# Kernel optimization log

Hardware: AMD Instinct MI355X
Metric: run time of the kernel (lower is better)

Reference implementation:

```python
import jax, jax.numpy as jnp
import numpy as np

NUM_BASE = 92
NUM_NOVEL = 40
GAMMA = 2.0
ALPHA = 0.25
DISTIL_FACTOR = 1.0
BSZ, N_DET, DIM_FEAT, DIM_HID, DIM_EMB = 16, 48, 2048, 1024, 512
EMB_HALF = DIM_EMB // 2


def _pair_ids(n):
    # all ordered pairs (i, j), i != j  (trajid2pairid)
    s, o = np.meshgrid(np.arange(n), np.arange(n), indexing='ij')
    m = s != o
    return s[m].astype(np.int32), o[m].astype(np.int32)


def _norm(x, eps=1e-12):
    # F.normalize(dim=-1)
    return x / jnp.maximum(jnp.linalg.norm(x, axis=-1, keepdims=True), eps)


def _sigmoid_focal_loss(logits, targets):
    # torchvision.ops.sigmoid_focal_loss, alpha=0.25, gamma=2, reduction='none'
    p = jax.nn.sigmoid(logits)
    ce = jnp.maximum(logits, 0) - logits * targets + jnp.log1p(jnp.exp(-jnp.abs(logits)))
    p_t = p * targets + (1.0 - p) * (1.0 - targets)
    loss = ce * (1.0 - p_t) ** GAMMA
    a_t = ALPHA * targets + (1.0 - ALPHA) * (1.0 - targets)
    return a_t * loss


def setup_inputs() -> dict:
    key = jax.random.key(0)
    ks = jax.random.split(key, 12)
    sids_np, oids_np = _pair_ids(N_DET)
    P = sids_np.shape[0]  # 2256 pairs per video
    w = lambda k, shape, s=0.02: jax.random.normal(k, shape, dtype=jnp.float32) * s
    return {
        'det_feats': jax.random.normal(ks[0], (BSZ, N_DET, DIM_FEAT), dtype=jnp.float32),
        'traj_embds': jax.random.normal(ks[1], (BSZ, N_DET, EMB_HALF), dtype=jnp.float32),
        'relpos_feats': jax.random.normal(ks[2], (BSZ, P, 12), dtype=jnp.float32),
        'classifier_weights': _norm(jax.random.normal(ks[3], (NUM_BASE, DIM_EMB), dtype=jnp.float32)) / np.sqrt(2.0),
        'W1': w(ks[4], (2 * DIM_FEAT, DIM_HID)), 'b1': jnp.zeros((DIM_HID,), jnp.float32),
        'W2': w(ks[5], (DIM_HID, DIM_HID)), 'b2': jnp.zeros((DIM_HID,), jnp.float32),
        'W3': w(ks[6], (DIM_HID, DIM_EMB)),
        'R1': w(ks[7], (12, 256), 0.1), 'rb1': jnp.zeros((256,), jnp.float32),
        'R2': w(ks[8], (256, DIM_EMB), 0.1),
        'temperature': jnp.full((1,), 0.02, dtype=jnp.float32),
        'labels': jax.random.randint(ks[9], (BSZ, P, 1 + NUM_BASE + NUM_NOVEL), 0, 2, dtype=jnp.int32),
        'sids': jnp.asarray(sids_np),
        'oids': jnp.asarray(oids_np),
    }


def reference(det_feats, traj_embds, relpos_feats, classifier_weights,
              W1, b1, W2, b2, W3, R1, rb1, R2, temperature,
              labels, sids, oids):
    Df = det_feats.shape[-1]
    De = traj_embds.shape[-1]
    # gather subject / object features for all pairs, flatten batch
    s_f = det_feats[:, sids, :].reshape(-1, Df)   # [N, Df]
    o_f = det_feats[:, oids, :].reshape(-1, Df)
    so = jnp.concatenate([s_f, o_f], axis=-1)      # [N, 2*Df]
    # trajpair_proj MLP
    h = jax.nn.relu(so @ W1 + b1)
    h = jax.nn.relu(h @ W2 + b2)
    so_proj = h @ W3                                # [N, dim_emb]
    so_n = _norm(so_proj)
    # relpos branch
    rp = relpos_feats.reshape(-1, relpos_feats.shape[-1])
    re = jax.nn.relu(rp @ R1 + rb1) @ R2
    re = _norm(re)
    combined = _norm(so_n + re)
    logits = (combined @ classifier_weights.T) / temperature  # [N, num_base]
    # cls_loss_on_base
    lab = labels.reshape(-1, 1 + NUM_BASE + NUM_NOVEL).astype(logits.dtype)
    pos_mask = jnp.any(lab[:, 1:1 + NUM_BASE] > 0, axis=-1)
    neg_mask = lab[:, 0] > 0
    lab_base = lab[:, 1:1 + NUM_BASE]
    fl_pos = _sigmoid_focal_loss(logits, lab_base)
    pos_den = jnp.maximum(pos_mask.sum(), 1).astype(logits.dtype) * NUM_BASE
    pos_loss = jnp.sum(fl_pos * pos_mask[:, None]) / pos_den
    fl_neg = _sigmoid_focal_loss(logits, jnp.zeros_like(logits))
    neg_den = jnp.maximum(neg_mask.sum(), 1).astype(logits.dtype) * NUM_BASE
    neg_loss = jnp.sum(fl_neg * neg_mask[:, None]) / neg_den
    # distillation L1 loss
    s_e = traj_embds[:, sids, :].reshape(-1, De)
    o_e = traj_embds[:, oids, :].reshape(-1, De)
    distil_target = jnp.concatenate([s_e, o_e], axis=-1)  # [N, dim_emb]
    distil_loss = jnp.mean(jnp.abs(distil_target - so_proj)) * DISTIL_FACTOR
    total_loss = pos_loss + neg_loss + distil_loss
    return total_loss
```

## Files before the change

### kernel.cpp

```cpp
#include <hip/hip_runtime.h>
#include <math.h>

constexpr int BSZ   = 16;
constexpr int NDET  = 48;
constexpr int PAIRS = NDET * (NDET - 1);
constexpr int ROWS  = BSZ * PAIRS;
constexpr int DF    = 2048;
constexpr int DH    = 1024;
constexpr int DE    = 512;
constexpr int EHALF = 256;
constexpr int NCLS  = 92;
constexpr int NEXT  = DE + 128;
constexpr int LABW  = 1 + 92 + 40;

typedef __attribute__((ext_vector_type(8))) short bf16x8;
typedef __attribute__((ext_vector_type(4))) float f32x4;

__device__ __forceinline__ short f2bf(float f) {
    union { float f; unsigned u; } a; a.f = f;
    unsigned r = a.u + 0x7fffu + ((a.u >> 16) & 1u);
    return (short)(r >> 16);
}
__device__ __forceinline__ float bf2f(short h) {
    union { unsigned u; float f; } x;
    x.u = ((unsigned)(unsigned short)h) << 16;
    return x.f;
}

constexpr int N4DET = BSZ * NDET * DF / 4;
constexpr int N4CWT = 128 * DE / 4;
constexpr int N4W3  = DH * DE / 4;
constexpr int N4R2  = 256 * DE / 4;
constexpr int NCONVB = (N4DET + N4CWT + N4W3 + N4R2) / 256;

struct TransJobs {
    const float* src[5];
    short*       dst[5];
    int K[5], N[5];
    int cum[6];
};

__global__ __launch_bounds__(256) void prep_kernel(
    const float* __restrict__ det, short* __restrict__ det_bf,
    const float* __restrict__ cw, short* __restrict__ cwt,
    const float* __restrict__ W3, short* __restrict__ W3bf,
    const float* __restrict__ R2, short* __restrict__ R2bf,
    TransJobs jobs)
{
    if (blockIdx.x < NCONVB) {
        int i = blockIdx.x * 256 + threadIdx.x;
        const float* src; short* dst; int k;
        if (i < N4DET) { src = det; dst = det_bf; k = i; }
        else if (i < N4DET + N4CWT) {
            k = i - N4DET;
            int n = (k * 4) >> 9;
            short4 o = {0, 0, 0, 0};
            if (n < NCLS) {
                float4 v = ((const float4*)cw)[k];
                o.x = f2bf(v.x); o.y = f2bf(v.y); o.z = f2bf(v.z); o.w = f2bf(v.w);
            }
            ((short4*)cwt)[k] = o;
            return;
        }
        else if (i < N4DET + N4CWT + N4W3) { src = W3; dst = W3bf; k = i - N4DET - N4CWT; }
        else { src = R2; dst = R2bf; k = i - N4DET - N4CWT - N4W3; }
        float4 v = ((const float4*)src)[k];
        short4 o;
        o.x = f2bf(v.x); o.y = f2bf(v.y); o.z = f2bf(v.z); o.w = f2bf(v.w);
        ((short4*)dst)[k] = o;
        return;
    }
    __shared__ float tile[32][33];
    int t = blockIdx.x - NCONVB;
    int j = 0;
    while (t >= jobs.cum[j + 1]) ++j;
    int lt = t - jobs.cum[j];
    int K = jobs.K[j], N = jobs.N[j];
    int nx = N >> 5;
    int ky = lt / nx, nxi = lt - ky * nx;
    int n0 = nxi * 32, k0 = ky * 32;
    const float* src = jobs.src[j];
    short* dst = jobs.dst[j];
    int tx = threadIdx.x & 31, ty = threadIdx.x >> 5;
#pragma unroll
    for (int i = ty; i < 32; i += 8)
        tile[i][tx] = src[(size_t)(k0 + i) * N + n0 + tx];
    __syncthreads();
#pragma unroll
    for (int i = ty; i < 32; i += 8)
        dst[(size_t)(n0 + i) * K + k0 + tx] = f2bf(tile[tx][i]);
}

__device__ __forceinline__ void load16_lds(const void* g, void* l) {
    __builtin_amdgcn_global_load_lds(
        (const __attribute__((address_space(1))) unsigned int*)g,
        (__attribute__((address_space(3))) unsigned int*)l, 16, 0, 0);
}

template <bool BIAS, bool RELU, bool OUTBF16, bool SWIZZLE, bool DUAL>
__global__ __launch_bounds__(256, 4) void mfma_gemm(
    const short* __restrict__ A, const short* __restrict__ Bt,
    const float* __restrict__ bias, void* __restrict__ C,
    int M, int N, int K, int lda, int ldb,
    const short* A2, const short* Bt2, void* C2, int nsplit,
    int K2, int lda2, int ldb2, int N2)
{
    __shared__ __align__(16) char smem_raw[32768];
    short* As = (short*)smem_raw;
    short* Bs = As + 128 * 64;

    int bx, by;
    if (SWIZZLE) {
        int nb  = gridDim.x;
        int gid = blockIdx.y * nb + blockIdx.x;
        int xcd = gid & 7;
        int j   = gid >> 3;
        int rows_per = gridDim.y >> 3;
        int lr  = j / nb;
        bx = j - lr * nb;
        by = xcd * rows_per + lr;
    } else {
        bx = blockIdx.x; by = blockIdx.y;
    }
    if (DUAL && bx >= nsplit) {
        bx -= nsplit; A = A2; Bt = Bt2; C = C2;
        K = K2; lda = lda2; ldb = ldb2; N = N2;
    }
    if (by * 128 >= M) return;

    const int tid  = threadIdx.x;
    const int wave = tid >> 6;
    const int lane = tid & 63;
    const int m0 = by * 128;
    const int n0 = bx * 128;
    const int wm = (wave & 1) * 64;
    const int wn = (wave >> 1) * 64;

    f32x4 acc[4][4] = {};

    const int q  = lane >> 4;
    const int lm = lane & 15;

    for (int k0 = 0; k0 < K; k0 += 64) {
#pragma unroll
        for (int it = 0; it < 4; ++it) {
            int c    = (it & 1) * 256 + tid;
            int half = it >> 1;
            int row  = c >> 2;
            int kk   = (c & 3) * 8 + half * 32;
            int ldsc = half * 4096 + ((it & 1) * 256 + wave * 64) * 8;
            int gm = m0 + row; if (gm >= M) gm = M - 1;
            load16_lds(A + (size_t)gm * lda + k0 + kk, As + ldsc);
            int gn = n0 + row;
            load16_lds(Bt + (size_t)gn * ldb + k0 + kk, Bs + ldsc);
        }
        __syncthreads();

#pragma unroll
        for (int half = 0; half < 2; ++half) {
            const short* Ah = As + half * 4096;
            const short* Bh = Bs + half * 4096;
            bf16x8 af[4], bfr[4];
#pragma unroll
            for (int t = 0; t < 4; ++t) {
                af[t]  = *(const bf16x8*)(Ah + (wm + t * 16 + lm) * 32 + q * 8);
                bfr[t] = *(const bf16x8*)(Bh + (wn + t * 16 + lm) * 32 + q * 8);
            }
#pragma unroll
            for (int tm = 0; tm < 4; ++tm)
#pragma unroll
                for (int tn = 0; tn < 4; ++tn)
                    acc[tm][tn] = __builtin_amdgcn_mfma_f32_16x16x32_bf16(
                        af[tm], bfr[tn], acc[tm][tn], 0, 0, 0);
        }
        __syncthreads();
    }

    if (OUTBF16) {
        float* scratch = (float*)smem_raw + wave * (16 * 68);
#pragma unroll
        for (int tm = 0; tm < 4; ++tm) {
            __syncthreads();
#pragma unroll
            for (int tn = 0; tn < 4; ++tn) {
                float bv = BIAS ? bias[n0 + wn + tn * 16 + lm] : 0.0f;
#pragma unroll
                for (int r = 0; r < 4; ++r) {
                    float v = acc[tm][tn][r] + bv;
                    if (RELU) v = fmaxf(v, 0.0f);
                    scratch[(q * 4 + r) * 68 + tn * 16 + lm] = v;
                }
            }
            __syncthreads();
#pragma unroll
            for (int p = 0; p < 2; ++p) {
                int row16 = (lane >> 3) + p * 8;
                int c0 = (lane & 7) * 8;
                float4 v0 = *(float4*)&scratch[row16 * 68 + c0];
                float4 v1 = *(float4*)&scratch[row16 * 68 + c0 + 4];
                bf16x8 o;
                o[0] = f2bf(v0.x); o[1] = f2bf(v0.y); o[2] = f2bf(v0.z); o[3] = f2bf(v0.w);
                o[4] = f2bf(v1.x); o[5] = f2bf(v1.y); o[6] = f2bf(v1.z); o[7] = f2bf(v1.w);
                int grow = m0 + wm + tm * 16 + row16;
                if (grow < M)
                    *(bf16x8*)((short*)C + (size_t)grow * N + n0 + wn + c0) = o;
            }
        }
    } else {
#pragma unroll
        for (int tm = 0; tm < 4; ++tm)
#pragma unroll
            for (int tn = 0; tn < 4; ++tn) {
                int col = n0 + wn + tn * 16 + lm;
#pragma unroll
                for (int r = 0; r < 4; ++r) {
                    int row = m0 + wm + tm * 16 + q * 4 + r;
                    if (row < M) {
                        float v = acc[tm][tn][r];
                        if (BIAS) v += bias[col];
                        if (RELU) v = fmaxf(v, 0.0f);
                        ((float*)C)[(size_t)row * N + col] = v;
                    }
                }
            }
    }
}

constexpr int N4UV = BSZ * NDET * 2048 / 4;
__global__ __launch_bounds__(256) void uvmerge_kernel(
    short* __restrict__ UVa, const short* __restrict__ UVb,
    const float* __restrict__ b1)
{
    int i = blockIdx.x * 256 + threadIdx.x;
    if (i >= N4UV) return;
    short4 a = ((const short4*)UVa)[i];
    short4 b = ((const short4*)UVb)[i];
    int col4 = i & 511;
    float4 bb = {0.0f, 0.0f, 0.0f, 0.0f};
    if (col4 < 256) bb = ((const float4*)b1)[col4];
    short4 o;
    o.x = f2bf(bf2f(a.x) + bf2f(b.x) + bb.x);
    o.y = f2bf(bf2f(a.y) + bf2f(b.y) + bb.y);
    o.z = f2bf(bf2f(a.z) + bf2f(b.z) + bb.z);
    o.w = f2bf(bf2f(a.w) + bf2f(b.w) + bb.w);
    ((short4*)UVa)[i] = o;
}

__global__ __launch_bounds__(256) void pairs_rh_kernel(
    const short* __restrict__ UVs,
    const int* __restrict__ sids, const int* __restrict__ oids,
    short* __restrict__ h1,
    const float* __restrict__ rp, const float* __restrict__ R1,
    const float* __restrict__ rb1, short* __restrict__ rh, int b0)
{
    int r = blockIdx.x;
    int b = b0 + r / PAIRS;
    int p = r % PAIRS;
    int j = threadIdx.x;

    size_t soff = (size_t)(b * NDET + sids[p]) * 2048;
    size_t ooff = (size_t)(b * NDET + oids[p]) * 2048 + 1024;
    short4 a1 = ((const short4*)(UVs + soff))[j];
    short4 a3 = ((const short4*)(UVs + ooff))[j];
    short4 h;
    h.x = f2bf(fmaxf(bf2f(a1.x) + bf2f(a3.x), 0.0f));
    h.y = f2bf(fmaxf(bf2f(a1.y) + bf2f(a3.y), 0.0f));
    h.z = f2bf(fmaxf(bf2f(a1.z) + bf2f(a3.z), 0.0f));
    h.w = f2bf(fmaxf(bf2f(a1.w) + bf2f(a3.w), 0.0f));
    ((short4*)(h1 + (size_t)r * DH))[j] = h;

    int rg = b0 * PAIRS + r;
    const float* row = rp + (size_t)rg * 12;
    float acc = rb1[j];
#pragma unroll
    for (int k = 0; k < 12; ++k) acc = fmaf(row[k], R1[k * 256 + j], acc);
    rh[(size_t)r * 256 + j] = f2bf(fmaxf(acc, 0.0f));
}

__global__ __launch_bounds__(256) void rowprep_focal_kernel(
    const short* __restrict__ so_ext, const short* __restrict__ re_ext,
    const float* __restrict__ traj, const float* __restrict__ temperature,
    const int* __restrict__ sids, const int* __restrict__ oids,
    const int* __restrict__ labels,
    float4* __restrict__ pn, float* __restrict__ dist_arr, int b0)
{
    int wave = threadIdx.x >> 6, lane = threadIdx.x & 63;
    int r = blockIdx.x * 4 + wave;
    int rg = b0 * PAIRS + r;
    int b = b0 + r / PAIRS;
    int p = r % PAIRS;

    const short* srow = so_ext + (size_t)r * NEXT;
    const short* rrow = re_ext + (size_t)r * NEXT;
    bf16x8 sv = *(const bf16x8*)(srow + lane * 8);
    bf16x8 uv = *(const bf16x8*)(rrow + lane * 8);
    float s[8], u[8];
#pragma unroll
    for (int i = 0; i < 8; ++i) { s[i] = bf2f(sv[i]); u[i] = bf2f(uv[i]); }

    const float* tsrc = (lane < 32)
        ? (traj + (size_t)(b * NDET + sids[p]) * EHALF + lane * 8)
        : (traj + (size_t)(b * NDET + oids[p]) * EHALF + (lane - 32) * 8);
    float4 t0 = ((const float4*)tsrc)[0], t1 = ((const float4*)tsrc)[1];
    float t[8] = {t0.x, t0.y, t0.z, t0.w, t1.x, t1.y, t1.z, t1.w};

    float ss = 0.0f, sr = 0.0f, rho = 0.0f, sd = 0.0f;
#pragma unroll
    for (int i = 0; i < 8; ++i) {
        ss  += s[i] * s[i];
        sr  += u[i] * u[i];
        rho += s[i] * u[i];
        sd  += fabsf(t[i] - s[i]);
    }
#pragma unroll
    for (int m = 1; m < 64; m <<= 1) {
        ss  += __shfl_xor(ss, m);
        sr  += __shfl_xor(sr, m);
        rho += __shfl_xor(rho, m);
        sd  += __shfl_xor(sd, m);
    }
    float inv_s = 1.0f / fmaxf(sqrtf(ss), 1e-12f);
    float inv_r = 1.0f / fmaxf(sqrtf(sr), 1e-12f);
    float ncomb = sqrtf(fmaxf(2.0f + 2.0f * rho * inv_s * inv_r, 0.0f));
    float scale = 1.0f / (fmaxf(ncomb, 1e-12f) * temperature[0]);

    float flp = 0.0f, fln = 0.0f, fm = 0.0f;
    size_t labbase = (size_t)rg * LABW;
#pragma unroll
    for (int h = 0; h < 2; ++h) {
        int c = lane + h * 64;
        if (c < NCLS) {
            float l = (bf2f(srow[DE + c]) * inv_s + bf2f(rrow[DE + c]) * inv_r) * scale;
            int tl = labels[labbase + 1 + c];
            if (tl > 0) fm = 1.0f;
            float tf = (float)tl;
            float pr = 1.0f / (1.0f + expf(-l));
            float lg = log1pf(expf(-fabsf(l)));
            float ce = fmaxf(l, 0.0f) - l * tf + lg;
            float pt = pr * tf + (1.0f - pr) * (1.0f - tf);
            float om = 1.0f - pt;
            float at = 0.25f * tf + 0.75f * (1.0f - tf);
            flp += at * ce * om * om;
            float ce0 = fmaxf(l, 0.0f) + lg;
            fln += 0.75f * ce0 * pr * pr;
        }
    }
#pragma unroll
    for (int m = 1; m < 64; m <<= 1) {
        flp += __shfl_xor(flp, m);
        fln += __shfl_xor(fln, m);
        fm  += __shfl_xor(fm, m);
    }
    if (lane == 0) {
        int posf = (fm > 0.5f) ? 1 : 0;
        int negf = (labels[labbase] > 0) ? 1 : 0;
        pn[rg] = make_float4(posf ? flp : 0.0f, negf ? fln : 0.0f, 0.0f,
                             (float)(posf + 2 * negf));
        dist_arr[rg] = sd;
    }
}

struct RedRec { double sp, sn, sd; int cp, cn; };
constexpr int RED1 = 64;
constexpr int ROWS_PER_RED = ROWS / RED1;

__global__ __launch_bounds__(256) void reduce1_kernel(
    const float4* __restrict__ pn, const float* __restrict__ dist_arr,
    RedRec* __restrict__ scratch)
{
    int tid = threadIdx.x;
    int base = blockIdx.x * ROWS_PER_RED;
    double sp = 0.0, sn = 0.0, sd = 0.0;
    int cp = 0, cn = 0;
    for (int i = tid; i < ROWS_PER_RED; i += 256) {
        float4 v = pn[base + i];
        sp += (double)v.x; sn += (double)v.y; sd += (double)dist_arr[base + i];
        int f = (int)v.w;
        cp += f & 1; cn += (f >> 1) & 1;
    }
    __shared__ double A[256], B[256], C[256];
    __shared__ int I[256], J[256];
    A[tid] = sp; B[tid] = sn; C[tid] = sd; I[tid] = cp; J[tid] = cn;
    __syncthreads();
    for (int st = 128; st > 0; st >>= 1) {
        if (tid < st) { A[tid] += A[tid + st]; B[tid] += B[tid + st]; C[tid] += C[tid + st];
                        I[tid] += I[tid + st]; J[tid] += J[tid + st]; }
        __syncthreads();
    }
    if (tid == 0) {
        RedRec rec; rec.sp = A[0]; rec.sn = B[0]; rec.sd = C[0];
        rec.cp = I[0]; rec.cn = J[0];
        scratch[blockIdx.x] = rec;
    }
}

__global__ __launch_bounds__(64) void reduce2_kernel(
    const RedRec* __restrict__ scratch, float* __restrict__ out)
{
    int lane = threadIdx.x;
    RedRec rec = scratch[lane];
    double sp = rec.sp, sn = rec.sn, sd = rec.sd;
    int cp = rec.cp, cn = rec.cn;
#pragma unroll
    for (int m = 1; m < 64; m <<= 1) {
        sp += __shfl_xor(sp, m);
        sn += __shfl_xor(sn, m);
        sd += __shfl_xor(sd, m);
        cp += __shfl_xor(cp, m);
        cn += __shfl_xor(cn, m);
    }
    if (lane == 0) {
        int cpv = cp < 1 ? 1 : cp;
        int cnv = cn < 1 ? 1 : cn;
        out[0] = (float)(sp / ((double)cpv * NCLS) +
                         sn / ((double)cnv * NCLS) +
                         sd / ((double)ROWS * DE));
    }
}

static inline int pad8(int x) { return (x + 7) & ~7; }

extern "C" void kernel_launch(void* const* d_in, const int* in_sizes, int n_in,
                              void* d_out, int out_size, void* d_ws, size_t ws_size,
                              hipStream_t stream)
{
    const float* det    = (const float*)d_in[0];
    const float* traj   = (const float*)d_in[1];
    const float* relpos = (const float*)d_in[2];
    const float* cw     = (const float*)d_in[3];
    const float* W1     = (const float*)d_in[4];
    const float* b1     = (const float*)d_in[5];
    const float* W2     = (const float*)d_in[6];
    const float* b2     = (const float*)d_in[7];
    const float* W3     = (const float*)d_in[8];
    const float* R1     = (const float*)d_in[9];
    const float* rb1    = (const float*)d_in[10];
    const float* R2     = (const float*)d_in[11];
    const float* temp   = (const float*)d_in[12];
    const int*   labels = (const int*)d_in[13];
    const int*   sids   = (const int*)d_in[14];
    const int*   oids   = (const int*)d_in[15];
    float* out = (float*)d_out;

    char* ws = (char*)d_ws;
    size_t off = 0;
    auto carve = [&](size_t bytes) -> char* {
        char* p = ws + off;
        off = (off + bytes + 255) & ~(size_t)255;
        return p;
    };
    float4* pn       = (float4*)carve((size_t)ROWS * 16);
    float*  dist_arr = (float*)carve((size_t)ROWS * 4);
    short*  det_bf   = (short*)carve((size_t)BSZ * NDET * DF * 2);
    short*  W1t      = (short*)carve((size_t)2048 * 2048 * 2);
    short*  W2t      = (short*)carve((size_t)DH * DH * 2);
    short*  W3t      = (short*)carve((size_t)NEXT * DH * 2);
    short*  R2t      = (short*)carve((size_t)NEXT * 256 * 2);
    short*  cwt      = (short*)carve((size_t)128 * DE * 2);
    short*  W3bf     = (short*)carve((size_t)DH * DE * 2);
    short*  R2bf     = (short*)carve((size_t)256 * DE * 2);
    short*  UVa      = (short*)carve((size_t)BSZ * NDET * 2048 * 2);
    short*  UVb      = (short*)carve((size_t)BSZ * NDET * 2048 * 2);
    RedRec* red_scratch = (RedRec*)carve((size_t)RED1 * sizeof(RedRec));
    size_t fixed_off = off;

    int b_ch = 1;
    for (int cand : {16, 8, 4, 2, 1}) {
        size_t rows  = (size_t)cand * PAIRS;
        size_t bytes = fixed_off + rows * 2048 + 256 + rows * 2048 + 256
                     + rows * 512 + 256 + rows * 1280 + 256;
        if (bytes <= ws_size) { b_ch = cand; break; }
    }
    const int chunk_rows = b_ch * PAIRS;
    const int n_chunks = BSZ / b_ch;
    char* reg1 = carve((size_t)chunk_rows * 2048);
    char* reg2 = carve((size_t)chunk_rows * 2048);
    char* reg3 = carve((size_t)chunk_rows * 512);
    char* reg4 = carve((size_t)chunk_rows * 1280);

    short* h1     = (short*)reg1;
    short* h2     = (short*)reg2;
    short* so_ext = (short*)reg1;
    short* rh     = (short*)reg3;
    short* re_ext = (short*)reg4;

    TransJobs tj;
    tj.src[0] = W1;                    tj.dst[0] = W1t;                   tj.K[0] = DF;  tj.N[0] = DH;
    tj.src[1] = W1 + (size_t)DF * DH;  tj.dst[1] = W1t + (size_t)DH * DF; tj.K[1] = DF;  tj.N[1] = DH;
    tj.src[2] = W2;                    tj.dst[2] = W2t;                   tj.K[2] = DH;  tj.N[2] = DH;
    tj.src[3] = W3;                    tj.dst[3] = W3t;                   tj.K[3] = DH;  tj.N[3] = DE;
    tj.src[4] = R2;                    tj.dst[4] = R2t;                   tj.K[4] = 256; tj.N[4] = DE;
    tj.cum[0] = 0;
    for (int i = 0; i < 5; ++i)
        tj.cum[i + 1] = tj.cum[i] + (tj.K[i] / 32) * (tj.N[i] / 32);
    prep_kernel<<<NCONVB + tj.cum[5], 256, 0, stream>>>(
        det, det_bf, cw, cwt, W3, W3bf, R2, R2bf, tj);

    mfma_gemm<false, false, true, false, true>
        <<<dim3(10, 1), 256, 0, stream>>>(
        cwt, W3bf, nullptr, W3t + (size_t)512 * DH, 128, 1024, 512, 512, 512,
        cwt, R2bf, R2t + (size_t)512 * 256, 8, 512, 512, 512, 256);

    mfma_gemm<false, false, true, false, true>
        <<<dim3(32, 6), 256, 0, stream>>>(
        det_bf, W1t, nullptr, UVa, BSZ * NDET, 2048, 1024, 2048, 2048,
        det_bf + 1024, W1t + 1024, UVb, 16, 1024, 2048, 2048, 2048);

    uvmerge_kernel<<<(N4UV + 255) / 256, 256, 0, stream>>>(UVa, UVb, b1);

    const int mg  = (chunk_rows + 127) / 128;
    const int mgp = pad8(mg);

    for (int c = 0; c < n_chunks; ++c) {
        int b0 = c * b_ch;
        int r0 = b0 * PAIRS;

        pairs_rh_kernel<<<chunk_rows, 256, 0, stream>>>(
            UVa, sids, oids, h1, relpos, R1, rb1, rh, b0);

        mfma_gemm<true, true, true, true, false>
            <<<dim3(DH / 128, mgp), 256, 0, stream>>>(
            h1, W2t, b2, h2, chunk_rows, DH, DH, DH, DH,
            nullptr, nullptr, nullptr, 0, 0, 0, 0, 0);

        mfma_gemm<false, false, true, true, true>
            <<<dim3(10, mgp), 256, 0, stream>>>(
            h2, W3t, nullptr, so_ext, chunk_rows, NEXT, DH, DH, DH,
            rh, R2t, re_ext, 5, 256, 256, 256, NEXT);

        rowprep_focal_kernel<<<chunk_rows / 4, 256, 0, stream>>>(
            so_ext, re_ext, traj, temp, sids, oids, labels, pn, dist_arr, b0);
    }

    reduce1_kernel<<<RED1, 256, 0, stream>>>(pn, dist_arr, red_scratch);
    reduce2_kernel<<<1, 64, 0, stream>>>(red_scratch, out);
}
```

Measured before the change: 388.4 us.

## Merge setup GEMMs into one multi-job launch and widen pairs kernel per wave

Replaces the two separate setup GEMM launches (classifier-projection and the W1 split products) with a single grouped GEMM kernel that dispatches blocks to four jobs. Its epilogue stages results through LDS so bf16 output is written as 16-byte rows. The pairs/relpos kernel is also changed to handle one row per wave with 16-byte vector loads instead of one row per 256-thread block. This cuts launch count, lets the small GEMMs fill otherwise idle CUs, and widens memory accesses, at the cost of a runtime job-lookup loop and added epilogue synchronisation.

After: 367.3 us, median of 2. -5.4%, faster.

```diff
diff --git a/kernel.cpp b/kernel.cpp
--- a/kernel.cpp
+++ b/kernel.cpp
@@ -226,6 +226,102 @@
     }
 }
 
+struct GemmJobs {
+    const short* A[4]; const short* Bt[4]; short* C[4];
+    int M[4], N[4], K[4], lda[4], ldb[4];
+    int cum[5];
+};
+
+__global__ __launch_bounds__(256, 4) void mfma_gemm_multi(GemmJobs jobs)
+{
+    __shared__ __align__(16) char smem_raw[32768];
+    short* As = (short*)smem_raw;
+    short* Bs = As + 128 * 64;
+
+    int bid = blockIdx.x;
+    int j = 0;
+    while (bid >= jobs.cum[j + 1]) ++j;
+    int lt = bid - jobs.cum[j];
+    const short* A  = jobs.A[j];
+    const short* Bt = jobs.Bt[j];
+    short* C = jobs.C[j];
+    int M = jobs.M[j], N = jobs.N[j], K = jobs.K[j];
+    int lda = jobs.lda[j], ldb = jobs.ldb[j];
+    int ncols = N >> 7;
+    int by = lt / ncols;
+    int bx = lt - by * ncols;
+
+    const int tid  = threadIdx.x;
+    const int wave = tid >> 6;
+    const int lane = tid & 63;
+    const int m0 = by * 128;
+    const int n0 = bx * 128;
+    const int wm = (wave & 1) * 64;
+    const int wn = (wave >> 1) * 64;
+
+    f32x4 acc[4][4] = {};
+    const int q  = lane >> 4;
+    const int lm = lane & 15;
+
+    for (int k0 = 0; k0 < K; k0 += 64) {
+#pragma unroll
+        for (int it = 0; it < 4; ++it) {
+            int c    = (it & 1) * 256 + tid;
+            int half = it >> 1;
+            int row  = c >> 2;
+            int kk   = (c & 3) * 8 + half * 32;
+            int ldsc = half * 4096 + ((it & 1) * 256 + wave * 64) * 8;
+            int gm = m0 + row; if (gm >= M) gm = M - 1;
+            load16_lds(A + (size_t)gm * lda + k0 + kk, As + ldsc);
+            load16_lds(Bt + (size_t)(n0 + row) * ldb + k0 + kk, Bs + ldsc);
+        }
+        __syncthreads();
+#pragma unroll
+        for (int half = 0; half < 2; ++half) {
+            const short* Ah = As + half * 4096;
+            const short* Bh = Bs + half * 4096;
+            bf16x8 af[4], bfr[4];
+#pragma unroll
+            for (int t = 0; t < 4; ++t) {
+                af[t]  = *(const bf16x8*)(Ah + (wm + t * 16 + lm) * 32 + q * 8);
+                bfr[t] = *(const bf16x8*)(Bh + (wn + t * 16 + lm) * 32 + q * 8);
+            }
+#pragma unroll
+            for (int tm = 0; tm < 4; ++tm)
+#pragma unroll
+                for (int tn = 0; tn < 4; ++tn)
+                    acc[tm][tn] = __builtin_amdgcn_mfma_f32_16x16x32_bf16(
+                        af[tm], bfr[tn], acc[tm][tn], 0, 0, 0);
+        }
+        __syncthreads();
+    }
+
+    float* scratch = (float*)smem_raw + wave * (16 * 68);
+#pragma unroll
+    for (int tm = 0; tm < 4; ++tm) {
+        __syncthreads();
+#pragma unroll
+        for (int tn = 0; tn < 4; ++tn)
+#pragma unroll
+            for (int r = 0; r < 4; ++r)
+                scratch[(q * 4 + r) * 68 + tn * 16 + lm] = acc[tm][tn][r];
+        __syncthreads();
+#pragma unroll
+        for (int p = 0; p < 2; ++p) {
+            int row16 = (lane >> 3) + p * 8;
+            int c0 = (lane & 7) * 8;
+            float4 v0 = *(float4*)&scratch[row16 * 68 + c0];
+            float4 v1 = *(float4*)&scratch[row16 * 68 + c0 + 4];
+            bf16x8 o;
+            o[0] = f2bf(v0.x); o[1] = f2bf(v0.y); o[2] = f2bf(v0.z); o[3] = f2bf(v0.w);
+            o[4] = f2bf(v1.x); o[5] = f2bf(v1.y); o[6] = f2bf(v1.z); o[7] = f2bf(v1.w);
+            int grow = m0 + wm + tm * 16 + row16;
+            if (grow < M)
+                *(bf16x8*)(C + (size_t)grow * N + n0 + wn + c0) = o;
+        }
+    }
+}
+
 constexpr int N4UV = BSZ * NDET * 2048 / 4;
 __global__ __launch_bounds__(256) void uvmerge_kernel(
     short* __restrict__ UVa, const short* __restrict__ UVb,
@@ -253,28 +349,43 @@
     const float* __restrict__ rp, const float* __restrict__ R1,
     const float* __restrict__ rb1, short* __restrict__ rh, int b0)
 {
-    int r = blockIdx.x;
+    int wave = threadIdx.x >> 6, lane = threadIdx.x & 63;
+    int r = blockIdx.x * 4 + wave;
     int b = b0 + r / PAIRS;
     int p = r % PAIRS;
-    int j = threadIdx.x;
-
-    size_t soff = (size_t)(b * NDET + sids[p]) * 2048;
-    size_t ooff = (size_t)(b * NDET + oids[p]) * 2048 + 1024;
-    short4 a1 = ((const short4*)(UVs + soff))[j];
-    short4 a3 = ((const short4*)(UVs + ooff))[j];
-    short4 h;
-    h.x = f2bf(fmaxf(bf2f(a1.x) + bf2f(a3.x), 0.0f));
-    h.y = f2bf(fmaxf(bf2f(a1.y) + bf2f(a3.y), 0.0f));
-    h.z = f2bf(fmaxf(bf2f(a1.z) + bf2f(a3.z), 0.0f));
-    h.w = f2bf(fmaxf(bf2f(a1.w) + bf2f(a3.w), 0.0f));
-    ((short4*)(h1 + (size_t)r * DH))[j] = h;
+
+    const bf16x8* us = (const bf16x8*)(UVs + (size_t)(b * NDET + sids[p]) * 2048);
+    const bf16x8* uo = (const bf16x8*)(UVs + (size_t)(b * NDET + oids[p]) * 2048 + 1024);
+    bf16x8* hrow = (bf16x8*)(h1 + (size_t)r * DH);
+#pragma unroll
+    for (int i = 0; i < 2; ++i) {
+        int idx = lane + i * 64;
+        bf16x8 a = us[idx], c = uo[idx];
+        bf16x8 h;
+#pragma unroll
+        for (int e = 0; e < 8; ++e)
+            h[e] = f2bf(fmaxf(bf2f(a[e]) + bf2f(c[e]), 0.0f));
+        hrow[idx] = h;
+    }
 
     int rg = b0 * PAIRS + r;
-    const float* row = rp + (size_t)rg * 12;
-    float acc = rb1[j];
-#pragma unroll
-    for (int k = 0; k < 12; ++k) acc = fmaf(row[k], R1[k * 256 + j], acc);
-    rh[(size_t)r * 256 + j] = f2bf(fmaxf(acc, 0.0f));
+    const float* rowp = rp + (size_t)rg * 12;
+    float4 acc = ((const float4*)rb1)[lane];
+#pragma unroll
+    for (int k = 0; k < 12; ++k) {
+        float rv = rowp[k];
+        float4 w = ((const float4*)(R1 + k * 256))[lane];
+        acc.x = fmaf(rv, w.x, acc.x);
+        acc.y = fmaf(rv, w.y, acc.y);
+        acc.z = fmaf(rv, w.z, acc.z);
+        acc.w = fmaf(rv, w.w, acc.w);
+    }
+    short4 o;
+    o.x = f2bf(fmaxf(acc.x, 0.0f));
+    o.y = f2bf(fmaxf(acc.y, 0.0f));
+    o.z = f2bf(fmaxf(acc.z, 0.0f));
+    o.w = f2bf(fmaxf(acc.w, 0.0f));
+    ((short4*)(rh + (size_t)r * 256))[lane] = o;
 }
 
 __global__ __launch_bounds__(256) void rowprep_focal_kernel(
@@ -496,15 +607,23 @@
     prep_kernel<<<NCONVB + tj.cum[5], 256, 0, stream>>>(
         det, det_bf, cw, cwt, W3, W3bf, R2, R2bf, tj);
 
-    mfma_gemm<false, false, true, false, true>
-        <<<dim3(10, 1), 256, 0, stream>>>(
-        cwt, W3bf, nullptr, W3t + (size_t)512 * DH, 128, 1024, 512, 512, 512,
-        cwt, R2bf, R2t + (size_t)512 * 256, 8, 512, 512, 512, 256);
-
-    mfma_gemm<false, false, true, false, true>
-        <<<dim3(32, 6), 256, 0, stream>>>(
-        det_bf, W1t, nullptr, UVa, BSZ * NDET, 2048, 1024, 2048, 2048,
-        det_bf + 1024, W1t + 1024, UVb, 16, 1024, 2048, 2048, 2048);
+    GemmJobs gj;
+    gj.A[0] = det_bf;        gj.Bt[0] = W1t;        gj.C[0] = UVa;
+    gj.M[0] = BSZ * NDET;    gj.N[0] = 2048;        gj.K[0] = 1024;
+    gj.lda[0] = 2048;        gj.ldb[0] = 2048;
+    gj.A[1] = det_bf + 1024; gj.Bt[1] = W1t + 1024; gj.C[1] = UVb;
+    gj.M[1] = BSZ * NDET;    gj.N[1] = 2048;        gj.K[1] = 1024;
+    gj.lda[1] = 2048;        gj.ldb[1] = 2048;
+    gj.A[2] = cwt;           gj.Bt[2] = W3bf;       gj.C[2] = W3t + (size_t)512 * DH;
+    gj.M[2] = 128;           gj.N[2] = 1024;        gj.K[2] = 512;
+    gj.lda[2] = 512;         gj.ldb[2] = 512;
+    gj.A[3] = cwt;           gj.Bt[3] = R2bf;       gj.C[3] = R2t + (size_t)512 * 256;
+    gj.M[3] = 128;           gj.N[3] = 256;         gj.K[3] = 512;
+    gj.lda[3] = 512;         gj.ldb[3] = 512;
+    gj.cum[0] = 0;
+    for (int i = 0; i < 4; ++i)
+        gj.cum[i + 1] = gj.cum[i] + (gj.N[i] / 128) * ((gj.M[i] + 127) / 128);
+    mfma_gemm_multi<<<gj.cum[4], 256, 0, stream>>>(gj);
 
     uvmerge_kernel<<<(N4UV + 255) / 256, 256, 0, stream>>>(UVa, UVb, b1);
 
@@ -513,9 +632,8 @@
 
     for (int c = 0; c < n_chunks; ++c) {
         int b0 = c * b_ch;
-        int r0 = b0 * PAIRS;
-
-        pairs_rh_kernel<<<chunk_rows, 256, 0, stream>>>(
+
+        pairs_rh_kernel<<<chunk_rows / 4, 256, 0, stream>>>(
             UVa, sids, oids, h1, relpos, R1, rb1, rh, b0);
 
         mfma_gemm<true, true, true, true, false>
```
